# Performance work log

Hardware: AMD Instinct MI355X
Metric: run time of the kernel (lower is better)

Reference implementation:

```python
import math
import jax, jax.numpy as jnp
import numpy as np

N_FLOWS = 5
DIM = 64
NH = 128          # hidden multiplier -> hidden width = DIM*NH = 8192
BATCH = 4096


def _masks(out_f, in_f, dim):
    od, idd = out_f // dim, in_f // dim
    mask_d = np.zeros((out_f, in_f), np.float32)
    mask_o = np.ones((out_f, in_f), np.float32)
    for i in range(dim):
        mask_d[i * od:(i + 1) * od, i * idd:(i + 1) * idd] = 1.0
        mask_o[i * od:(i + 1) * od, i * idd:] = 0.0
    return jnp.asarray(mask_d), jnp.asarray(mask_o)

MASK_D1, MASK_O1 = _masks(DIM * NH, DIM, DIM)   # layer 1: (H, D)
MASK_D2, MASK_O2 = _masks(DIM, DIM * NH, DIM)   # layer 2: (D, H)


def masked_weight(x, W, dw, b, mask_d, mask_o, dim, grad=None):
    """MaskedWeight.forward. W:(out,in), dw:(out,1), b:(out,)."""
    out_f, in_f = W.shape
    od, idd = out_f // dim, in_f // dim
    w = jnp.exp(W) * mask_d + W * mask_o                 # (out, in)
    wsn = jnp.sum(w * w, axis=-1, keepdims=True)         # (out, 1)
    wn = jnp.exp(dw) * w / jnp.sqrt(wsn)                 # weight-normalized
    wpl = dw + W - 0.5 * jnp.log(wsn)                    # (out, in)
    # extract diagonal blocks of wpl^T: (dim, idd, od)
    blocks = wpl.reshape(dim, od, dim, idd)
    wpl_t = blocks[np.arange(dim), :, np.arange(dim), :].transpose(0, 2, 1)
    y = x @ wn.T + b                                     # (B, out)
    g = wpl_t.transpose(0, 2, 1)                         # (dim, od, idd)
    if grad is None:
        new_grad = jnp.broadcast_to(g[None], (x.shape[0],) + g.shape)
    else:
        # logsumexp over contracted block axis: out (B, dim, od, b_prev)
        new_grad = jax.nn.logsumexp(
            g[None, :, :, None, :] + jnp.swapaxes(grad, -2, -1)[:, :, None, :, :],
            axis=-1)
    return y, new_grad


def tanh_layer(x, grad):
    g = -2.0 * (x - math.log(2.0) + jax.nn.softplus(-2.0 * x))
    return jnp.tanh(x), g.reshape(grad.shape) + grad


def bnaf_flow(x, W1, d1, b1, W2, d2, b2, gate):
    h, g = masked_weight(x, W1, d1, b1, MASK_D1, MASK_O1, DIM)
    h, g = tanh_layer(h, g)
    y, g = masked_weight(h, W2, d2, b2, MASK_D2, MASK_O2, DIM, grad=g)
    grad = g[:, :, 0, 0]                                  # (B, DIM) -- squeeze
    if gate is None:                                      # res=None (last flow)
        return y, jnp.sum(grad, axis=-1)
    s = jax.nn.sigmoid(gate)                              # res='gated'
    out = s * y + (1.0 - s) * x
    ld = jnp.sum(jax.nn.softplus(grad + gate) - jax.nn.softplus(gate), axis=-1)
    return out, ld


def setup_inputs() -> dict:
    key = jax.random.key(0)
    ks = jax.random.split(key, 8)
    H = DIM * NH
    return {
        "x":  jax.random.normal(ks[0], (BATCH, DIM), jnp.float32),
        "W1": jax.random.normal(ks[1], (N_FLOWS, H, DIM), jnp.float32) * 0.1,
        "d1": jax.random.normal(ks[2], (N_FLOWS, H, 1), jnp.float32) * 0.1,
        "b1": jax.random.normal(ks[3], (N_FLOWS, H), jnp.float32) * 0.01,
        "W2": jax.random.normal(ks[4], (N_FLOWS, DIM, H), jnp.float32) * 0.1,
        "d2": jax.random.normal(ks[5], (N_FLOWS, DIM, 1), jnp.float32) * 0.1,
        "b2": jax.random.normal(ks[6], (N_FLOWS, DIM), jnp.float32) * 0.01,
        "gates": jax.random.normal(ks[7], (N_FLOWS - 1,), jnp.float32),
    }


def reference(x, W1, d1, b1, W2, d2, b2, gates):
    log_det = jnp.zeros(x.shape[0], x.dtype)
    for f in range(N_FLOWS):
        gate = gates[f] if f < N_FLOWS - 1 else None
        x, ld = bnaf_flow(x, W1[f], d1[f], b1[f], W2[f], d2[f], b2[f], gate)
        log_det = log_det + ld
        if f < N_FLOWS - 1:                               # Permutation 'flip'
            x = x[:, ::-1]
    return x, log_det
```

## Files before the change

### kernel.cpp

```cpp
#include <hip/hip_runtime.h>
#include <hip/hip_bf16.h>
#include <math.h>

#define NFLOWS 5
#define DIMF 64
#define HID 8192
#define BATCHN 4096

typedef unsigned int u32;
typedef __bf16 bf16x8 __attribute__((ext_vector_type(8)));
typedef float f32x4 __attribute__((ext_vector_type(4)));

__device__ __forceinline__ short f2bf_s(float x){
  u32 b = __float_as_uint(x);
  b += 0x7fff + ((b >> 16) & 1);
  return (short)(b >> 16);
}
__device__ __forceinline__ u32 pk_bf16(float a, float b){
#if __has_builtin(__builtin_amdgcn_cvt_pk_bf16_f32)
  typedef __bf16 bf16x2_t __attribute__((ext_vector_type(2)));
  bf16x2_t r = __builtin_amdgcn_cvt_pk_bf16_f32(a, b);
  return __builtin_bit_cast(u32, r);
#else
  u32 x = __float_as_uint(a); x += 0x7fff + ((x >> 16) & 1);
  u32 y = __float_as_uint(b); y += 0x7fff + ((y >> 16) & 1);
  return (x >> 16) | (y & 0xffff0000u);
#endif
}
__device__ __forceinline__ float softplus_f(float z){
  return fmaxf(z, 0.f) + log1pf(__expf(-fabsf(z)));
}

__global__ __launch_bounds__(1024) void prep_fused_kernel(
    const float* __restrict__ W1, const float* __restrict__ d1,
    const float* __restrict__ W2, const float* __restrict__ d2,
    short* __restrict__ wn1s, short* __restrict__ wn2s,
    float* __restrict__ expc4, float* __restrict__ cmax)
{
  __shared__ float scl[128];
  __shared__ float g1s[128];
  __shared__ float cbuf[128];
  __shared__ float red[16];
  __shared__ float Msh;

  const int tid  = threadIdx.x;
  const int w    = tid >> 6;
  const int lane = tid & 63;
  const int f    = blockIdx.x >> 6;
  const int i    = blockIdx.x & 63;

  #pragma unroll
  for (int it = 0; it < 8; ++it) {
    int rr = w * 8 + it;
    size_t R = (size_t)(f * HID + i * 128 + rr);
    float Wv = W1[R * 64 + lane];
    float wv = (lane == i) ? __expf(Wv) : ((lane < i) ? Wv : 0.f);
    float sq = wv * wv;
    #pragma unroll
    for (int m = 1; m < 64; m <<= 1) sq += __shfl_xor(sq, m, 64);
    float d1v = d1[R];
    if (lane == 0) scl[rr] = __expf(d1v) * rsqrtf(sq);
    if (lane == i) g1s[rr] = d1v + Wv - 0.5f * __logf(sq);
  }
  __syncthreads();

  {
    const int c   = tid >> 6;
    const int nt  = c >> 1, ks2 = c & 1;
    const int n16 = lane & 15, q4 = lane >> 4;
    const int row = nt * 16 + n16;
    const int k0  = ks2 * 32 + q4 * 8;
    const float* src = W1 + ((size_t)(f * HID + i * 128 + row)) * 64 + k0;
    float4 a = *(const float4*)src;
    float4 b = *(const float4*)(src + 4);
    float wv[8] = {a.x, a.y, a.z, a.w, b.x, b.y, b.z, b.w};
    float sc = scl[row];
    #pragma unroll
    for (int e = 0; e < 8; ++e) {
      int k = k0 + e;
      float v = (k == i) ? __expf(wv[e]) : ((k < i) ? wv[e] : 0.f);
      wv[e] = v * sc;
    }
    uint4 pk4;
    pk4.x = pk_bf16(wv[0], wv[1]); pk4.y = pk_bf16(wv[2], wv[3]);
    pk4.z = pk_bf16(wv[4], wv[5]); pk4.w = pk_bf16(wv[6], wv[7]);
    short* dstp = wn1s + ((((size_t)(f * 64 + i) * 8 + nt) * 2 + ks2) << 9)
                + lane * 8;
    *(uint4*)dstp = pk4;
  }

  const float* Wrow = W2 + ((size_t)(f * DIMF + i)) * HID;
  const float d2v = d2[f * DIMF + i];
  const int k0 = tid * 8;
  const int kb = tid >> 4;
  float4 a = *(const float4*)(Wrow + k0);
  float4 b = *(const float4*)(Wrow + k0 + 4);
  float wv[8] = {a.x, a.y, a.z, a.w, b.x, b.y, b.z, b.w};
  const bool diag = (kb == i);
  float cv[8];
  float mv[8];
  #pragma unroll
  for (int e = 0; e < 8; ++e) {
    if (diag)        { cv[e] = g1s[(k0 - i * 128) + e] + d2v + wv[e]; mv[e] = __expf(wv[e]); }
    else if (kb > i) { mv[e] = 0.f; }
    else             { mv[e] = wv[e]; }
  }
  float part = 0.f;
  #pragma unroll
  for (int e = 0; e < 8; ++e) part = fmaf(mv[e], mv[e], part);
  #pragma unroll
  for (int m = 1; m < 64; m <<= 1) part += __shfl_xor(part, m, 64);
  if (lane == 0) red[w] = part;
  __syncthreads();
  float wsn = 0.f;
  #pragma unroll
  for (int e = 0; e < 16; ++e) wsn += red[e];
  float ls = __logf(wsn);
  float sc2 = __expf(d2v) * rsqrtf(wsn);

  if (diag) {
    int rr0 = k0 - i * 128;
    #pragma unroll
    for (int e = 0; e < 8; ++e) cbuf[rr0 + e] = cv[e] - 0.5f * ls;
  }
  {
    int ks = (k0 >> 5) & 3, qq = (k0 >> 3) & 3;
    int mt2 = i >> 4, c16r = i & 15;
    size_t dst = ((((size_t)(f * 64 + kb) * 4 + ks) * 4 + mt2) << 9)
               + ((qq * 16 + c16r) << 3);
    uint4 pk4;
    pk4.x = pk_bf16(mv[0]*sc2, mv[1]*sc2); pk4.y = pk_bf16(mv[2]*sc2, mv[3]*sc2);
    pk4.z = pk_bf16(mv[4]*sc2, mv[5]*sc2); pk4.w = pk_bf16(mv[6]*sc2, mv[7]*sc2);
    *(uint4*)(wn2s + dst) = pk4;
  }
  __syncthreads();

  if (w == 0) {
    float m = fmaxf(cbuf[lane], cbuf[lane + 64]);
    #pragma unroll
    for (int s = 1; s < 64; s <<= 1) m = fmaxf(m, __shfl_xor(m, s, 64));
    if (lane == 0) { cmax[f * DIMF + i] = m; Msh = m; }
  }
  __syncthreads();
  if (tid < 128) expc4[f * HID + i * 128 + tid] = 4.f * __expf(cbuf[tid] - Msh);
}

__global__ __launch_bounds__(1024, 4)
void bnaf_main_kernel(
    const float* __restrict__ x_in,
    const float* __restrict__ b1, const float* __restrict__ b2,
    const float* __restrict__ gates,
    const short* __restrict__ wn1s,
    const short* __restrict__ wn2s,
    const float* __restrict__ expc4, const float* __restrict__ cmax,
    float* __restrict__ out)
{
  __shared__ __attribute__((aligned(16))) char smem[146816];
  float* xs  = (float*)smem;
  short* xbS = (short*)(smem + 4352);
  float* ldp = (float*)(smem + 145792);

  const int tid  = threadIdx.x;
  const int w    = tid >> 6;
  const int lane = tid & 63;
  const int c16  = lane & 15;
  const int q    = lane >> 4;
  const int r0   = blockIdx.x * 16;

  short* tbuf0 = (short*)(smem + 6528 + w * 8704);
  short* tbuf1 = (short*)(smem + 6528 + w * 8704 + 4352);

  {
    int row = tid >> 6, col = tid & 63;
    float v = x_in[((size_t)(r0 + row) << 6) | col];
    xs[row * 68 + col] = v;
    xbS[(col >> 3) * 136 + row * 8 + (col & 7)] = f2bf_s(v);
  }
  float ldtot = 0.f;
  __syncthreads();

  #pragma unroll 1
  for (int f = 0; f < NFLOWS; ++f) {
    const float gatev = (f < NFLOWS - 1) ? gates[f] : 0.f;
    const float spg   = (f < NFLOWS - 1) ? softplus_f(gatev) : 0.f;

    const bf16x8 xa0 = *(const bf16x8*)(xbS + q * 136 + c16 * 8);
    const bf16x8 xa1 = *(const bf16x8*)(xbS + (4 + q) * 136 + c16 * 8);

    f32x4 yacc[4];
    #pragma unroll
    for (int n = 0; n < 4; ++n) yacc[n] = f32x4{0.f, 0.f, 0.f, 0.f};
    float ldacc = 0.f;

    #pragma unroll 1
    for (int ii = 0; ii < 4; ++ii) {
      const int i = ii * 16 + w;
      short* tb = (ii & 1) ? tbuf1 : tbuf0;
      const short* p1l = wn1s + (((size_t)(f * 64 + i)) << 13) + lane * 8;
      const float* b1p = b1    + f * HID + i * 128 + q * 4;
      const float* ecp = expc4 + f * HID + i * 128 + q * 4;
      const bool hiHalf = (i >= 32);

      float s0 = 0.f, s1 = 0.f;
      f32x4 dd[4];

      #pragma unroll
      for (int nt = 0; nt < 4; ++nt) {
        float4 b1q = *(const float4*)(b1p + nt * 16);
        f32x4 z = {b1q.x, b1q.y, b1q.z, b1q.w};
        bf16x8 bw0 = *(const bf16x8*)(p1l + nt * 1024);
        dd[nt] = __builtin_amdgcn_mfma_f32_16x16x32_bf16(bw0, xa0, z, 0, 0, 0);
      }
      if (hiHalf) {
        #pragma unroll
        for (int nt = 0; nt < 4; ++nt) {
          bf16x8 bw1 = *(const bf16x8*)(p1l + nt * 1024 + 512);
          dd[nt] = __builtin_amdgcn_mfma_f32_16x16x32_bf16(bw1, xa1, dd[nt], 0, 0, 0);
        }
      }
      #pragma unroll
      for (int nt = 0; nt < 4; ++nt) {
        float4 ecq = *(const float4*)(ecp + nt * 16);
        float t[4];
        #pragma unroll
        for (int r = 0; r < 4; ++r) {
          float ee = (r == 0) ? ecq.x : (r == 1) ? ecq.y : (r == 2) ? ecq.z : ecq.w;
          float h  = dd[nt][r];
          float up = __expf(-2.f * fabsf(h));
          float vp = __builtin_amdgcn_rcpf(1.f + up);
          float ta = fmaf(-2.f * up, vp, 1.f);
          t[r] = copysignf(ta, h);
          float c1 = ee * up, c2 = vp * vp;
          if (r & 1) s1 = fmaf(c1, c2, s1); else s0 = fmaf(c1, c2, s0);
        }
        uint2 pk; pk.x = pk_bf16(t[0], t[1]); pk.y = pk_bf16(t[2], t[3]);
        *(uint2*)(tb + c16 * 136 + nt * 16 + q * 4) = pk;
      }

      if (ii > 0) {
        const int ip = i - 16;
        short* tp = ((ii - 1) & 1) ? tbuf1 : tbuf0;
        __builtin_amdgcn_sched_barrier(0);
        asm volatile("s_waitcnt lgkmcnt(0)" ::: "memory");
        const short* p2l = wn2s + (((size_t)(f * 64 + ip)) << 13) + lane * 8;
        const int mt0 = ip >> 4;
        #pragma unroll
        for (int ks = 0; ks < 4; ++ks) {
          if (ks == 2) __builtin_amdgcn_sched_barrier(0);
          bf16x8 tfrag = *(const bf16x8*)(tp + c16 * 136 + ks * 32 + q * 8);
          #pragma unroll
          for (int mt = 0; mt < 4; ++mt) {
            if (mt >= mt0) {
              bf16x8 wb = *(const bf16x8*)(p2l + (ks * 4 + mt) * 512);
              yacc[mt] = __builtin_amdgcn_mfma_f32_16x16x32_bf16(wb, tfrag, yacc[mt], 0, 0, 0);
            }
          }
        }
        __builtin_amdgcn_sched_barrier(0);
      }

      #pragma unroll
      for (int nt = 0; nt < 4; ++nt) {
        float4 b1q = *(const float4*)(b1p + (nt + 4) * 16);
        f32x4 z = {b1q.x, b1q.y, b1q.z, b1q.w};
        bf16x8 bw0 = *(const bf16x8*)(p1l + (nt + 4) * 1024);
        dd[nt] = __builtin_amdgcn_mfma_f32_16x16x32_bf16(bw0, xa0, z, 0, 0, 0);
      }
      if (hiHalf) {
        #pragma unroll
        for (int nt = 0; nt < 4; ++nt) {
          bf16x8 bw1 = *(const bf16x8*)(p1l + (nt + 4) * 1024 + 512);
          dd[nt] = __builtin_amdgcn_mfma_f32_16x16x32_bf16(bw1, xa1, dd[nt], 0, 0, 0);
        }
      }
      #pragma unroll
      for (int nt = 0; nt < 4; ++nt) {
        float4 ecq = *(const float4*)(ecp + (nt + 4) * 16);
        float t[4];
        #pragma unroll
        for (int r = 0; r < 4; ++r) {
          float ee = (r == 0) ? ecq.x : (r == 1) ? ecq.y : (r == 2) ? ecq.z : ecq.w;
          float h  = dd[nt][r];
          float up = __expf(-2.f * fabsf(h));
          float vp = __builtin_amdgcn_rcpf(1.f + up);
          float ta = fmaf(-2.f * up, vp, 1.f);
          t[r] = copysignf(ta, h);
          float c1 = ee * up, c2 = vp * vp;
          if (r & 1) s1 = fmaf(c1, c2, s1); else s0 = fmaf(c1, c2, s0);
        }
        uint2 pk; pk.x = pk_bf16(t[0], t[1]); pk.y = pk_bf16(t[2], t[3]);
        *(uint2*)(tb + c16 * 136 + (nt + 4) * 16 + q * 4) = pk;
      }

      float sacc = s0 + s1;
      sacc += __shfl_xor(sacc, 16, 64);
      sacc += __shfl_xor(sacc, 32, 64);
      const float Mi = cmax[f * DIMF + i];
      float grad = Mi + __logf(sacc);
      ldacc += (f < NFLOWS - 1) ? (softplus_f(grad + gatev) - spg) : grad;
    }

    {
      const int ip = 48 + w;
      __builtin_amdgcn_sched_barrier(0);
      asm volatile("s_waitcnt lgkmcnt(0)" ::: "memory");
      const short* p2l = wn2s + (((size_t)(f * 64 + ip)) << 13) + lane * 8;
      const int mt0 = ip >> 4;
      #pragma unroll
      for (int ks = 0; ks < 4; ++ks) {
        if (ks == 2) __builtin_amdgcn_sched_barrier(0);
        bf16x8 tfrag = *(const bf16x8*)(tbuf1 + c16 * 136 + ks * 32 + q * 8);
        #pragma unroll
        for (int mt = 0; mt < 4; ++mt) {
          if (mt >= mt0) {
            bf16x8 wb = *(const bf16x8*)(p2l + (ks * 4 + mt) * 512);
            yacc[mt] = __builtin_amdgcn_mfma_f32_16x16x32_bf16(wb, tfrag, yacc[mt], 0, 0, 0);
          }
        }
      }
      __builtin_amdgcn_sched_barrier(0);
    }

    float* ypw = (float*)(smem + 6528 + w * 8704);
    #pragma unroll
    for (int mt = 0; mt < 4; ++mt)
      #pragma unroll
      for (int r = 0; r < 4; ++r)
        ypw[(mt * 4 + r) * 65 + lane] = yacc[mt][r];
    if (q == 0) ldp[w * 16 + c16] = ldacc;
    __syncthreads();

    float sgate = 0.f;
    if (f < NFLOWS - 1) sgate = __builtin_amdgcn_rcpf(1.f + __expf(-gatev));
    int row = tid >> 6, col = tid & 63;
    int idx = ((col >> 4) * 4 + (col & 3)) * 65 + (((col >> 2) & 3) * 16 + row);
    float v = b2[f * DIMF + col];
    #pragma unroll
    for (int ww = 0; ww < 16; ++ww)
      v += ((const float*)(smem + 6528 + ww * 8704))[idx];
    float nx = 0.f; int nrow = 0, ncol = 0;
    if (f < NFLOWS - 1) {
      float xv = xs[row * 68 + col];
      nx = fmaf(sgate, v - xv, xv);
      nrow = row; ncol = 63 - col;
    } else {
      out[((size_t)(r0 + row) << 6) | col] = v;
    }
    if (tid < 16) {
      float a = 0.f;
      #pragma unroll
      for (int ww = 0; ww < 16; ++ww) a += ldp[ww * 16 + tid];
      ldtot += a;
    }
    __syncthreads();
    if (f < NFLOWS - 1) {
      xs[nrow * 68 + ncol] = nx;
      xbS[(ncol >> 3) * 136 + nrow * 8 + (ncol & 7)] = f2bf_s(nx);
      __syncthreads();
    }
  }

  if (tid < 16) out[(size_t)BATCHN * DIMF + r0 + tid] = ldtot;
}

extern "C" void kernel_launch(void* const* d_in, const int* in_sizes, int n_in,
                              void* d_out, int out_size, void* d_ws, size_t ws_size,
                              hipStream_t stream)
{
  const float* x     = (const float*)d_in[0];
  const float* W1    = (const float*)d_in[1];
  const float* d1    = (const float*)d_in[2];
  const float* b1    = (const float*)d_in[3];
  const float* W2    = (const float*)d_in[4];
  const float* d2    = (const float*)d_in[5];
  const float* b2    = (const float*)d_in[6];
  const float* gates = (const float*)d_in[7];
  float* out = (float*)d_out;

  char* ws = (char*)d_ws;
  short* wn1s  = (short*)ws;
  short* wn2s  = (short*)(ws + 5242880);
  float* expc4 = (float*)(ws + 10485760);
  float* cmaxp = (float*)(ws + 10649600);

  hipLaunchKernelGGL(prep_fused_kernel, dim3(320), dim3(1024), 0, stream,
                     W1, d1, W2, d2, wn1s, wn2s, expc4, cmaxp);
  hipLaunchKernelGGL(bnaf_main_kernel, dim3(256), dim3(1024), 0, stream,
                     x, b1, b2, gates, wn1s, wn2s, expc4, cmaxp, out);
}
```

Measured before the change: 262.9 us.

## Specialize warps into layer-1 producers and layer-2 consumers with block-level pipelining

Waves 0-7 now compute only the first masked layer plus tanh for 8 hidden blocks each, and write bf16 activations into shared buffers. Waves 8-15 consume those buffers one step behind and run the second-layer MFMAs. A __syncthreads separates each of the 9 pipeline steps, and shared memory shrinks to about 75 KB. The aim is to overlap the exp-heavy layer-1 work with layer-2 matrix ops across waves and to cut LDS use, which may raise occupancy. In exchange it adds block-wide barriers at every step and leaves each wave group idle on alternate kinds of work, which can unbalance the load.

```diff
diff --git a/kernel.cpp b/kernel.cpp
--- a/kernel.cpp
+++ b/kernel.cpp
@@ -155,10 +155,11 @@
     const float* __restrict__ expc4, const float* __restrict__ cmax,
     float* __restrict__ out)
 {
-  __shared__ __attribute__((aligned(16))) char smem[146816];
+  __shared__ __attribute__((aligned(16))) char smem[76672];
   float* xs  = (float*)smem;
   short* xbS = (short*)(smem + 4352);
-  float* ldp = (float*)(smem + 145792);
+  short* tbufs = (short*)(smem + 6528);
+  float* ldp = (float*)(smem + 76160);
 
   const int tid  = threadIdx.x;
   const int w    = tid >> 6;
@@ -166,9 +167,8 @@
   const int c16  = lane & 15;
   const int q    = lane >> 4;
   const int r0   = blockIdx.x * 16;
-
-  short* tbuf0 = (short*)(smem + 6528 + w * 8704);
-  short* tbuf1 = (short*)(smem + 6528 + w * 8704 + 4352);
+  const bool isG1 = (w < 8);
+  const int g    = w & 7;
 
   {
     int row = tid >> 6, col = tid & 63;
@@ -184,151 +184,136 @@
     const float gatev = (f < NFLOWS - 1) ? gates[f] : 0.f;
     const float spg   = (f < NFLOWS - 1) ? softplus_f(gatev) : 0.f;
 
-    const bf16x8 xa0 = *(const bf16x8*)(xbS + q * 136 + c16 * 8);
-    const bf16x8 xa1 = *(const bf16x8*)(xbS + (4 + q) * 136 + c16 * 8);
-
+    bf16x8 xa0, xa1;
+    if (isG1) {
+      xa0 = *(const bf16x8*)(xbS + q * 136 + c16 * 8);
+      xa1 = *(const bf16x8*)(xbS + (4 + q) * 136 + c16 * 8);
+    }
     f32x4 yacc[4];
     #pragma unroll
     for (int n = 0; n < 4; ++n) yacc[n] = f32x4{0.f, 0.f, 0.f, 0.f};
     float ldacc = 0.f;
 
     #pragma unroll 1
-    for (int ii = 0; ii < 4; ++ii) {
-      const int i = ii * 16 + w;
-      short* tb = (ii & 1) ? tbuf1 : tbuf0;
-      const short* p1l = wn1s + (((size_t)(f * 64 + i)) << 13) + lane * 8;
-      const float* b1p = b1    + f * HID + i * 128 + q * 4;
-      const float* ecp = expc4 + f * HID + i * 128 + q * 4;
-      const bool hiHalf = (i >= 32);
-
-      float s0 = 0.f, s1 = 0.f;
-      f32x4 dd[4];
-
-      #pragma unroll
-      for (int nt = 0; nt < 4; ++nt) {
-        float4 b1q = *(const float4*)(b1p + nt * 16);
-        f32x4 z = {b1q.x, b1q.y, b1q.z, b1q.w};
-        bf16x8 bw0 = *(const bf16x8*)(p1l + nt * 1024);
-        dd[nt] = __builtin_amdgcn_mfma_f32_16x16x32_bf16(bw0, xa0, z, 0, 0, 0);
-      }
-      if (hiHalf) {
-        #pragma unroll
-        for (int nt = 0; nt < 4; ++nt) {
-          bf16x8 bw1 = *(const bf16x8*)(p1l + nt * 1024 + 512);
-          dd[nt] = __builtin_amdgcn_mfma_f32_16x16x32_bf16(bw1, xa1, dd[nt], 0, 0, 0);
+    for (int k = 0; k < 9; ++k) {
+      if (isG1) {
+        if (k < 8) {
+          const int grp = ((k & 1) << 2) | (k >> 1);
+          const int i = grp * 8 + g;
+          short* tb = tbufs + (g * 2 + (k & 1)) * 2176;
+          const short* p1l = wn1s + (((size_t)(f * 64 + i)) << 13) + lane * 8;
+          const float* b1p = b1    + f * HID + i * 128 + q * 4;
+          const float* ecp = expc4 + f * HID + i * 128 + q * 4;
+          const bool hiHalf = (k & 1);
+
+          float s0 = 0.f, s1 = 0.f;
+          f32x4 dd[4];
+
+          #pragma unroll
+          for (int nt = 0; nt < 4; ++nt) {
+            float4 b1q = *(const float4*)(b1p + nt * 16);
+            f32x4 z = {b1q.x, b1q.y, b1q.z, b1q.w};
+            bf16x8 bw0 = *(const bf16x8*)(p1l + nt * 1024);
+            dd[nt] = __builtin_amdgcn_mfma_f32_16x16x32_bf16(bw0, xa0, z, 0, 0, 0);
+          }
+          if (hiHalf) {
+            #pragma unroll
+            for (int nt = 0; nt < 4; ++nt) {
+              bf16x8 bw1 = *(const bf16x8*)(p1l + nt * 1024 + 512);
+              dd[nt] = __builtin_amdgcn_mfma_f32_16x16x32_bf16(bw1, xa1, dd[nt], 0, 0, 0);
+            }
+          }
+          #pragma unroll
+          for (int nt = 0; nt < 4; ++nt) {
+            float4 ecq = *(const float4*)(ecp + nt * 16);
+            float t[4];
+            #pragma unroll
+            for (int r = 0; r < 4; ++r) {
+              float ee = (r == 0) ? ecq.x : (r == 1) ? ecq.y : (r == 2) ? ecq.z : ecq.w;
+              float h  = dd[nt][r];
+              float up = __expf(-2.f * fabsf(h));
+              float vp = __builtin_amdgcn_rcpf(1.f + up);
+              float ta = fmaf(-2.f * up, vp, 1.f);
+              t[r] = copysignf(ta, h);
+              float c1 = ee * up, c2 = vp * vp;
+              if (r & 1) s1 = fmaf(c1, c2, s1); else s0 = fmaf(c1, c2, s0);
+            }
+            uint2 pk; pk.x = pk_bf16(t[0], t[1]); pk.y = pk_bf16(t[2], t[3]);
+            *(uint2*)(tb + c16 * 136 + nt * 16 + q * 4) = pk;
+          }
+
+          #pragma unroll
+          for (int nt = 0; nt < 4; ++nt) {
+            float4 b1q = *(const float4*)(b1p + (nt + 4) * 16);
+            f32x4 z = {b1q.x, b1q.y, b1q.z, b1q.w};
+            bf16x8 bw0 = *(const bf16x8*)(p1l + (nt + 4) * 1024);
+            dd[nt] = __builtin_amdgcn_mfma_f32_16x16x32_bf16(bw0, xa0, z, 0, 0, 0);
+          }
+          if (hiHalf) {
+            #pragma unroll
+            for (int nt = 0; nt < 4; ++nt) {
+              bf16x8 bw1 = *(const bf16x8*)(p1l + (nt + 4) * 1024 + 512);
+              dd[nt] = __builtin_amdgcn_mfma_f32_16x16x32_bf16(bw1, xa1, dd[nt], 0, 0, 0);
+            }
+          }
+          #pragma unroll
+          for (int nt = 0; nt < 4; ++nt) {
+            float4 ecq = *(const float4*)(ecp + (nt + 4) * 16);
+            float t[4];
+            #pragma unroll
+            for (int r = 0; r < 4; ++r) {
+              float ee = (r == 0) ? ecq.x : (r == 1) ? ecq.y : (r == 2) ? ecq.z : ecq.w;
+              float h  = dd[nt][r];
+              float up = __expf(-2.f * fabsf(h));
+              float vp = __builtin_amdgcn_rcpf(1.f + up);
+              float ta = fmaf(-2.f * up, vp, 1.f);
+              t[r] = copysignf(ta, h);
+              float c1 = ee * up, c2 = vp * vp;
+              if (r & 1) s1 = fmaf(c1, c2, s1); else s0 = fmaf(c1, c2, s0);
+            }
+            uint2 pk; pk.x = pk_bf16(t[0], t[1]); pk.y = pk_bf16(t[2], t[3]);
+            *(uint2*)(tb + c16 * 136 + (nt + 4) * 16 + q * 4) = pk;
+          }
+
+          float sacc = s0 + s1;
+          sacc += __shfl_xor(sacc, 16, 64);
+          sacc += __shfl_xor(sacc, 32, 64);
+          const float Mi = cmax[f * DIMF + i];
+          float grad = Mi + __logf(sacc);
+          ldacc += (f < NFLOWS - 1) ? (softplus_f(grad + gatev) - spg) : grad;
+        } else {
+          if (q == 0) ldp[g * 16 + c16] = ldacc;
+        }
+      } else {
+        if (k > 0) {
+          const int grp = (((k - 1) & 1) << 2) | ((k - 1) >> 1);
+          const int ip = grp * 8 + g;
+          const short* tp = tbufs + (g * 2 + ((k - 1) & 1)) * 2176;
+          const short* p2l = wn2s + (((size_t)(f * 64 + ip)) << 13) + lane * 8;
+          const int mt0 = grp >> 1;
+          #pragma unroll
+          for (int ks = 0; ks < 4; ++ks) {
+            bf16x8 tfrag = *(const bf16x8*)(tp + c16 * 136 + ks * 32 + q * 8);
+            #pragma unroll
+            for (int mt = 0; mt < 4; ++mt) {
+              if (mt >= mt0) {
+                bf16x8 wb = *(const bf16x8*)(p2l + (ks * 4 + mt) * 512);
+                yacc[mt] = __builtin_amdgcn_mfma_f32_16x16x32_bf16(wb, tfrag, yacc[mt], 0, 0, 0);
+              }
+            }
+          }
+          if (k == 8) {
+            float* ypw = (float*)(smem + 6528 + g * 8704);
+            #pragma unroll
+            for (int mt = 0; mt < 4; ++mt)
+              #pragma unroll
+              for (int r = 0; r < 4; ++r)
+                ypw[(mt * 4 + r) * 65 + lane] = yacc[mt][r];
+          }
         }
       }
-      #pragma unroll
-      for (int nt = 0; nt < 4; ++nt) {
-        float4 ecq = *(const float4*)(ecp + nt * 16);
-        float t[4];
-        #pragma unroll
-        for (int r = 0; r < 4; ++r) {
-          float ee = (r == 0) ? ecq.x : (r == 1) ? ecq.y : (r == 2) ? ecq.z : ecq.w;
-          float h  = dd[nt][r];
-          float up = __expf(-2.f * fabsf(h));
-          float vp = __builtin_amdgcn_rcpf(1.f + up);
-          float ta = fmaf(-2.f * up, vp, 1.f);
-          t[r] = copysignf(ta, h);
-          float c1 = ee * up, c2 = vp * vp;
-          if (r & 1) s1 = fmaf(c1, c2, s1); else s0 = fmaf(c1, c2, s0);
-        }
-        uint2 pk; pk.x = pk_bf16(t[0], t[1]); pk.y = pk_bf16(t[2], t[3]);
-        *(uint2*)(tb + c16 * 136 + nt * 16 + q * 4) = pk;
-      }
-
-      if (ii > 0) {
-        const int ip = i - 16;
-        short* tp = ((ii - 1) & 1) ? tbuf1 : tbuf0;
-        __builtin_amdgcn_sched_barrier(0);
-        asm volatile("s_waitcnt lgkmcnt(0)" ::: "memory");
-        const short* p2l = wn2s + (((size_t)(f * 64 + ip)) << 13) + lane * 8;
-        const int mt0 = ip >> 4;
-        #pragma unroll
-        for (int ks = 0; ks < 4; ++ks) {
-          if (ks == 2) __builtin_amdgcn_sched_barrier(0);
-          bf16x8 tfrag = *(const bf16x8*)(tp + c16 * 136 + ks * 32 + q * 8);
-          #pragma unroll
-          for (int mt = 0; mt < 4; ++mt) {
-            if (mt >= mt0) {
-              bf16x8 wb = *(const bf16x8*)(p2l + (ks * 4 + mt) * 512);
-              yacc[mt] = __builtin_amdgcn_mfma_f32_16x16x32_bf16(wb, tfrag, yacc[mt], 0, 0, 0);
-            }
-          }
-        }
-        __builtin_amdgcn_sched_barrier(0);
-      }
-
-      #pragma unroll
-      for (int nt = 0; nt < 4; ++nt) {
-        float4 b1q = *(const float4*)(b1p + (nt + 4) * 16);
-        f32x4 z = {b1q.x, b1q.y, b1q.z, b1q.w};
-        bf16x8 bw0 = *(const bf16x8*)(p1l + (nt + 4) * 1024);
-        dd[nt] = __builtin_amdgcn_mfma_f32_16x16x32_bf16(bw0, xa0, z, 0, 0, 0);
-      }
-      if (hiHalf) {
-        #pragma unroll
-        for (int nt = 0; nt < 4; ++nt) {
-          bf16x8 bw1 = *(const bf16x8*)(p1l + (nt + 4) * 1024 + 512);
-          dd[nt] = __builtin_amdgcn_mfma_f32_16x16x32_bf16(bw1, xa1, dd[nt], 0, 0, 0);
-        }
-      }
-      #pragma unroll
-      for (int nt = 0; nt < 4; ++nt) {
-        float4 ecq = *(const float4*)(ecp + (nt + 4) * 16);
-        float t[4];
-        #pragma unroll
-        for (int r = 0; r < 4; ++r) {
-          float ee = (r == 0) ? ecq.x : (r == 1) ? ecq.y : (r == 2) ? ecq.z : ecq.w;
-          float h  = dd[nt][r];
-          float up = __expf(-2.f * fabsf(h));
-          float vp = __builtin_amdgcn_rcpf(1.f + up);
-          float ta = fmaf(-2.f * up, vp, 1.f);
-          t[r] = copysignf(ta, h);
-          float c1 = ee * up, c2 = vp * vp;
-          if (r & 1) s1 = fmaf(c1, c2, s1); else s0 = fmaf(c1, c2, s0);
-        }
-        uint2 pk; pk.x = pk_bf16(t[0], t[1]); pk.y = pk_bf16(t[2], t[3]);
-        *(uint2*)(tb + c16 * 136 + (nt + 4) * 16 + q * 4) = pk;
-      }
-
-      float sacc = s0 + s1;
-      sacc += __shfl_xor(sacc, 16, 64);
-      sacc += __shfl_xor(sacc, 32, 64);
-      const float Mi = cmax[f * DIMF + i];
-      float grad = Mi + __logf(sacc);
-      ldacc += (f < NFLOWS - 1) ? (softplus_f(grad + gatev) - spg) : grad;
-    }
-
-    {
-      const int ip = 48 + w;
-      __builtin_amdgcn_sched_barrier(0);
-      asm volatile("s_waitcnt lgkmcnt(0)" ::: "memory");
-      const short* p2l = wn2s + (((size_t)(f * 64 + ip)) << 13) + lane * 8;
-      const int mt0 = ip >> 4;
-      #pragma unroll
-      for (int ks = 0; ks < 4; ++ks) {
-        if (ks == 2) __builtin_amdgcn_sched_barrier(0);
-        bf16x8 tfrag = *(const bf16x8*)(tbuf1 + c16 * 136 + ks * 32 + q * 8);
-        #pragma unroll
-        for (int mt = 0; mt < 4; ++mt) {
-          if (mt >= mt0) {
-            bf16x8 wb = *(const bf16x8*)(p2l + (ks * 4 + mt) * 512);
-            yacc[mt] = __builtin_amdgcn_mfma_f32_16x16x32_bf16(wb, tfrag, yacc[mt], 0, 0, 0);
-          }
-        }
-      }
-      __builtin_amdgcn_sched_barrier(0);
-    }
-
-    float* ypw = (float*)(smem + 6528 + w * 8704);
-    #pragma unroll
-    for (int mt = 0; mt < 4; ++mt)
-      #pragma unroll
-      for (int r = 0; r < 4; ++r)
-        ypw[(mt * 4 + r) * 65 + lane] = yacc[mt][r];
-    if (q == 0) ldp[w * 16 + c16] = ldacc;
-    __syncthreads();
+      __syncthreads();
+    }
 
     float sgate = 0.f;
     if (f < NFLOWS - 1) sgate = __builtin_amdgcn_rcpf(1.f + __expf(-gatev));
@@ -336,7 +321,7 @@
     int idx = ((col >> 4) * 4 + (col & 3)) * 65 + (((col >> 2) & 3) * 16 + row);
     float v = b2[f * DIMF + col];
     #pragma unroll
-    for (int ww = 0; ww < 16; ++ww)
+    for (int ww = 0; ww < 8; ++ww)
       v += ((const float*)(smem + 6528 + ww * 8704))[idx];
     float nx = 0.f; int nrow = 0, ncol = 0;
     if (f < NFLOWS - 1) {
@@ -349,7 +334,7 @@
     if (tid < 16) {
       float a = 0.f;
       #pragma unroll
-      for (int ww = 0; ww < 16; ++ww) a += ldp[ww * 16 + tid];
+      for (int ww = 0; ww < 8; ++ww) a += ldp[ww * 16 + tid];
       ldtot += a;
     }
     __syncthreads();
```

Measured after the change: 299.5 us. +13.9%, slower.

## Drop double-buffered layer-2 pipelining to halve LDS footprint per block

Applied to the files above, without the earlier changes.

Each wave now keeps a single bf16 tanh tile buffer instead of two, and runs the layer-2 MFMA accumulation right after computing the current hidden block. Previously that accumulation was deferred by one iteration and drained in an epilogue. Shared memory per block roughly halves, which could let two 1024-thread blocks fit on a CU. The cost is losing the software overlap between layer-1 transcendental work and layer-2 MFMAs inside each wave. With 256 blocks, the extra occupancy may not be used.

```diff
diff --git a/kernel.cpp b/kernel.cpp
--- a/kernel.cpp
+++ b/kernel.cpp
@@ -155,10 +155,10 @@
     const float* __restrict__ expc4, const float* __restrict__ cmax,
     float* __restrict__ out)
 {
-  __shared__ __attribute__((aligned(16))) char smem[146816];
+  __shared__ __attribute__((aligned(16))) char smem[77184];
   float* xs  = (float*)smem;
   short* xbS = (short*)(smem + 4352);
-  float* ldp = (float*)(smem + 145792);
+  float* ldp = (float*)(smem + 76160);
 
   const int tid  = threadIdx.x;
   const int w    = tid >> 6;
@@ -167,8 +167,7 @@
   const int q    = lane >> 4;
   const int r0   = blockIdx.x * 16;
 
-  short* tbuf0 = (short*)(smem + 6528 + w * 8704);
-  short* tbuf1 = (short*)(smem + 6528 + w * 8704 + 4352);
+  short* tw = (short*)(smem + 6528 + w * 4352);
 
   {
     int row = tid >> 6, col = tid & 63;
@@ -195,7 +194,6 @@
     #pragma unroll 1
     for (int ii = 0; ii < 4; ++ii) {
       const int i = ii * 16 + w;
-      short* tb = (ii & 1) ? tbuf1 : tbuf0;
       const short* p1l = wn1s + (((size_t)(f * 64 + i)) << 13) + lane * 8;
       const float* b1p = b1    + f * HID + i * 128 + q * 4;
       const float* ecp = expc4 + f * HID + i * 128 + q * 4;
@@ -234,29 +232,7 @@
           if (r & 1) s1 = fmaf(c1, c2, s1); else s0 = fmaf(c1, c2, s0);
         }
         uint2 pk; pk.x = pk_bf16(t[0], t[1]); pk.y = pk_bf16(t[2], t[3]);
-        *(uint2*)(tb + c16 * 136 + nt * 16 + q * 4) = pk;
-      }
-
-      if (ii > 0) {
-        const int ip = i - 16;
-        short* tp = ((ii - 1) & 1) ? tbuf1 : tbuf0;
-        __builtin_amdgcn_sched_barrier(0);
-        asm volatile("s_waitcnt lgkmcnt(0)" ::: "memory");
-        const short* p2l = wn2s + (((size_t)(f * 64 + ip)) << 13) + lane * 8;
-        const int mt0 = ip >> 4;
-        #pragma unroll
-        for (int ks = 0; ks < 4; ++ks) {
-          if (ks == 2) __builtin_amdgcn_sched_barrier(0);
-          bf16x8 tfrag = *(const bf16x8*)(tp + c16 * 136 + ks * 32 + q * 8);
-          #pragma unroll
-          for (int mt = 0; mt < 4; ++mt) {
-            if (mt >= mt0) {
-              bf16x8 wb = *(const bf16x8*)(p2l + (ks * 4 + mt) * 512);
-              yacc[mt] = __builtin_amdgcn_mfma_f32_16x16x32_bf16(wb, tfrag, yacc[mt], 0, 0, 0);
-            }
-          }
-        }
-        __builtin_amdgcn_sched_barrier(0);
+        *(uint2*)(tw + c16 * 136 + nt * 16 + q * 4) = pk;
       }
 
       #pragma unroll
@@ -289,7 +265,7 @@
           if (r & 1) s1 = fmaf(c1, c2, s1); else s0 = fmaf(c1, c2, s0);
         }
         uint2 pk; pk.x = pk_bf16(t[0], t[1]); pk.y = pk_bf16(t[2], t[3]);
-        *(uint2*)(tb + c16 * 136 + (nt + 4) * 16 + q * 4) = pk;
+        *(uint2*)(tw + c16 * 136 + (nt + 4) * 16 + q * 4) = pk;
       }
 
       float sacc = s0 + s1;
@@ -298,30 +274,27 @@
       const float Mi = cmax[f * DIMF + i];
       float grad = Mi + __logf(sacc);
       ldacc += (f < NFLOWS - 1) ? (softplus_f(grad + gatev) - spg) : grad;
-    }
-
-    {
-      const int ip = 48 + w;
-      __builtin_amdgcn_sched_barrier(0);
+
       asm volatile("s_waitcnt lgkmcnt(0)" ::: "memory");
-      const short* p2l = wn2s + (((size_t)(f * 64 + ip)) << 13) + lane * 8;
-      const int mt0 = ip >> 4;
-      #pragma unroll
-      for (int ks = 0; ks < 4; ++ks) {
-        if (ks == 2) __builtin_amdgcn_sched_barrier(0);
-        bf16x8 tfrag = *(const bf16x8*)(tbuf1 + c16 * 136 + ks * 32 + q * 8);
-        #pragma unroll
-        for (int mt = 0; mt < 4; ++mt) {
-          if (mt >= mt0) {
-            bf16x8 wb = *(const bf16x8*)(p2l + (ks * 4 + mt) * 512);
-            yacc[mt] = __builtin_amdgcn_mfma_f32_16x16x32_bf16(wb, tfrag, yacc[mt], 0, 0, 0);
+      {
+        const short* p2l = wn2s + (((size_t)(f * 64 + i)) << 13) + lane * 8;
+        const int mt0 = i >> 4;
+        #pragma unroll
+        for (int ks = 0; ks < 4; ++ks) {
+          bf16x8 tfrag = *(const bf16x8*)(tw + c16 * 136 + ks * 32 + q * 8);
+          #pragma unroll
+          for (int mt = 0; mt < 4; ++mt) {
+            if (mt >= mt0) {
+              bf16x8 wb = *(const bf16x8*)(p2l + (ks * 4 + mt) * 512);
+              yacc[mt] = __builtin_amdgcn_mfma_f32_16x16x32_bf16(wb, tfrag, yacc[mt], 0, 0, 0);
+            }
           }
         }
       }
-      __builtin_amdgcn_sched_barrier(0);
-    }
-
-    float* ypw = (float*)(smem + 6528 + w * 8704);
+    }
+
+    asm volatile("s_waitcnt lgkmcnt(0)" ::: "memory");
+    float* ypw = (float*)(smem + 6528 + w * 4352);
     #pragma unroll
     for (int mt = 0; mt < 4; ++mt)
       #pragma unroll
@@ -337,7 +310,7 @@
     float v = b2[f * DIMF + col];
     #pragma unroll
     for (int ww = 0; ww < 16; ++ww)
-      v += ((const float*)(smem + 6528 + ww * 8704))[idx];
+      v += ((const float*)(smem + 6528 + ww * 4352))[idx];
     float nx = 0.f; int nrow = 0, ncol = 0;
     if (f < NFLOWS - 1) {
       float xv = xs[row * 68 + col];
```

New measurement: 264.4 us. About the same (+0.5%).
